# Performance work log

Measured on AMD Instinct MI355X. Metric: run time of the kernel, lower is better.

## Reference

```python
import jax, jax.numpy as jnp
import numpy as np


def setup_inputs() -> dict:
    key = jax.random.key(0)
    kq, kv = jax.random.split(key)
    N, To, Ti, H = 8, 1024, 4096, 512
    queries = jax.random.normal(kq, (N, To, H), dtype=jnp.float32)
    values = jax.random.normal(kv, (N, Ti, H), dtype=jnp.float32)
    return {"queries": queries, "values": values}


def reference(queries, values):
    # scores: N x To x Ti (unscaled, unmasked dot-product attention)
    scores = jnp.einsum("noh,nih->noi", queries, values)
    attn = jax.nn.softmax(scores, axis=-1)          # softmax over Ti
    out = jnp.einsum("noi,nih->noh", attn, values)  # N x To x H
    return out, attn
```

## Files before the change

### kernel.cpp

```cpp
#include <hip/hip_runtime.h>
#include <hip/hip_bf16.h>

typedef __bf16 bf16x8 __attribute__((ext_vector_type(8)));
typedef __bf16 bf16x4 __attribute__((ext_vector_type(4)));
typedef float  f32x4  __attribute__((ext_vector_type(4)));

constexpr int N_  = 8;
constexpr int TO_ = 1024;
constexpr int TI_ = 4096;
constexpr int H_  = 512;

__device__ inline void split8(const float4& x0, const float4& x1,
                              bf16x8& h, bf16x8& l)
{
    float xs[8] = {x0.x, x0.y, x0.z, x0.w, x1.x, x1.y, x1.z, x1.w};
#pragma unroll
    for (int i = 0; i < 8; ++i) {
        __bf16 hh = (__bf16)xs[i];
        h[i] = hh;
        l[i] = (__bf16)(xs[i] - (float)hh);
    }
}

__device__ inline void cvt8(const float4& x0, const float4& x1, bf16x8& h)
{
    float xs[8] = {x0.x, x0.y, x0.z, x0.w, x1.x, x1.y, x1.z, x1.w};
#pragma unroll
    for (int i = 0; i < 8; ++i) h[i] = (__bf16)xs[i];
}

__global__ __launch_bounds__(256)
void zero_kernel(float4* __restrict__ p)
{
    p[(size_t)blockIdx.x * 256 + threadIdx.x] = float4{0.f, 0.f, 0.f, 0.f};
}

__global__ __launch_bounds__(256)
void split_kernel(const float* __restrict__ X, __bf16* __restrict__ Xh,
                  __bf16* __restrict__ Xl)
{
    const size_t idx = ((size_t)blockIdx.x * 256 + threadIdx.x) * 8;
    const float4* src = reinterpret_cast<const float4*>(X + idx);
    float4 x0 = src[0], x1 = src[1];
    bf16x8 h, l;
    split8(x0, x1, h, l);
    *reinterpret_cast<bf16x8*>(Xh + idx) = h;
    *reinterpret_cast<bf16x8*>(Xl + idx) = l;
}

__global__ __launch_bounds__(256)
void vt2_kernel(const __bf16* __restrict__ Vh, __bf16* __restrict__ Vt)
{
    const int hb = blockIdx.x, tb = blockIdx.y, n = blockIdx.z;
    const int h  = hb * 64 + (threadIdx.x >> 2);
    const int tq = threadIdx.x & 3;
    const __bf16* Vn = Vh + (size_t)n * TI_ * H_;
    __bf16* Vtn = Vt + (size_t)n * H_ * TI_;

#pragma unroll
    for (int j = 0; j < 16; ++j) {
        const int t0 = tb * 512 + tq * 128 + j * 8;
        bf16x8 o;
#pragma unroll
        for (int e = 0; e < 8; ++e)
            o[e] = Vn[(size_t)(t0 + e) * H_ + h];
        *reinterpret_cast<bf16x8*>(&Vtn[(size_t)h * TI_ + t0]) = o;
    }
}

constexpr int QLP = 40;

__global__ __launch_bounds__(256, 3)
void qk2_kernel(const __bf16* __restrict__ Qh, const __bf16* __restrict__ Ql,
                const __bf16* __restrict__ Vh, const __bf16* __restrict__ Vl,
                float* __restrict__ S)
{
    __shared__ __bf16 Ah[128 * QLP];
    __shared__ __bf16 Al[128 * QLP];
    __shared__ __bf16 Bh[128 * QLP];
    __shared__ __bf16 Bl[128 * QLP];

    const int tt = blockIdx.x, mt = blockIdx.y, n = blockIdx.z;
    const size_t qoff = ((size_t)n * TO_ + (size_t)mt * 128) * H_;
    const size_t voff = ((size_t)n * TI_ + (size_t)tt * 128) * H_;
    const __bf16* Qhb = Qh + qoff;
    const __bf16* Qlb = Ql + qoff;
    const __bf16* Vhb = Vh + voff;
    const __bf16* Vlb = Vl + voff;

    const int tid  = threadIdx.x;
    const int lane = tid & 63, wave = tid >> 6;
    const int wr = wave >> 1, wc = wave & 1;

    const int sr = tid >> 1;
    const int sc = (tid & 1) * 16;

    bf16x8 pAh[2], pAl[2], pBh[2], pBl[2];
    auto loadT = [&](int k0) {
#pragma unroll
        for (int c = 0; c < 2; ++c) {
            const size_t o = (size_t)sr * H_ + k0 + sc + c * 8;
            pAh[c] = *reinterpret_cast<const bf16x8*>(Qhb + o);
            pAl[c] = *reinterpret_cast<const bf16x8*>(Qlb + o);
            pBh[c] = *reinterpret_cast<const bf16x8*>(Vhb + o);
            pBl[c] = *reinterpret_cast<const bf16x8*>(Vlb + o);
        }
    };

    f32x4 acc[4][4] = {};
    const int fr = lane & 15, fg = (lane >> 4) * 8;

    loadT(0);
    for (int kt = 0; kt < 16; ++kt) {
        __syncthreads();
#pragma unroll
        for (int c = 0; c < 2; ++c) {
            const int o = sr * QLP + sc + c * 8;
            *reinterpret_cast<bf16x8*>(&Ah[o]) = pAh[c];
            *reinterpret_cast<bf16x8*>(&Al[o]) = pAl[c];
            *reinterpret_cast<bf16x8*>(&Bh[o]) = pBh[c];
            *reinterpret_cast<bf16x8*>(&Bl[o]) = pBl[c];
        }
        __syncthreads();
        if (kt + 1 < 16) loadT((kt + 1) * 32);

        bf16x8 bh[4], bl[4];
#pragma unroll
        for (int j = 0; j < 4; ++j) {
            const int row = wc * 64 + j * 16 + fr;
            bh[j] = *reinterpret_cast<const bf16x8*>(&Bh[row * QLP + fg]);
            bl[j] = *reinterpret_cast<const bf16x8*>(&Bl[row * QLP + fg]);
        }
#pragma unroll
        for (int m = 0; m < 4; ++m) {
            const int row = wr * 64 + m * 16 + fr;
            bf16x8 ah = *reinterpret_cast<const bf16x8*>(&Ah[row * QLP + fg]);
            bf16x8 al = *reinterpret_cast<const bf16x8*>(&Al[row * QLP + fg]);
#pragma unroll
            for (int j = 0; j < 4; ++j) {
                acc[m][j] = __builtin_amdgcn_mfma_f32_16x16x32_bf16(ah, bh[j], acc[m][j], 0, 0, 0);
                acc[m][j] = __builtin_amdgcn_mfma_f32_16x16x32_bf16(ah, bl[j], acc[m][j], 0, 0, 0);
                acc[m][j] = __builtin_amdgcn_mfma_f32_16x16x32_bf16(al, bh[j], acc[m][j], 0, 0, 0);
            }
        }
    }

    float* Sb = S + ((size_t)n * TO_ + (size_t)mt * 128) * TI_ + (size_t)tt * 128;
    const int crow0 = wr * 64 + (lane >> 4) * 4;
    const int ccol0 = wc * 64 + (lane & 15);
#pragma unroll
    for (int m = 0; m < 4; ++m)
#pragma unroll
        for (int j = 0; j < 4; ++j)
#pragma unroll
            for (int r = 0; r < 4; ++r)
                Sb[(size_t)(crow0 + m * 16 + r) * TI_ + (ccol0 + j * 16)] = acc[m][j][r];
}

__global__ __launch_bounds__(256)
void softmax2_kernel(float* __restrict__ S, __bf16* __restrict__ A16)
{
    const int wave = threadIdx.x >> 6, lane = threadIdx.x & 63;
    const size_t row = (size_t)blockIdx.x * 4 + wave;
    float4* p = reinterpret_cast<float4*>(S + row * TI_);
    __bf16* p16 = A16 + row * TI_;

    float4 v[16];
    float m = -3.0e38f;
#pragma unroll
    for (int j = 0; j < 16; ++j) {
        v[j] = p[j * 64 + lane];
        m = fmaxf(m, fmaxf(fmaxf(v[j].x, v[j].y), fmaxf(v[j].z, v[j].w)));
    }
#pragma unroll
    for (int s = 32; s > 0; s >>= 1) m = fmaxf(m, __shfl_xor(m, s));

    constexpr float L2E = 1.4426950408889634f;
    float sum = 0.f;
#pragma unroll
    for (int j = 0; j < 16; ++j) {
        v[j].x = exp2f((v[j].x - m) * L2E);
        v[j].y = exp2f((v[j].y - m) * L2E);
        v[j].z = exp2f((v[j].z - m) * L2E);
        v[j].w = exp2f((v[j].w - m) * L2E);
        sum += (v[j].x + v[j].y) + (v[j].z + v[j].w);
    }
#pragma unroll
    for (int s = 32; s > 0; s >>= 1) sum += __shfl_xor(sum, s);

    const float inv = 1.0f / sum;
#pragma unroll
    for (int j = 0; j < 16; ++j) {
        v[j].x *= inv; v[j].y *= inv; v[j].z *= inv; v[j].w *= inv;
        p[j * 64 + lane] = v[j];
        bf16x4 o;
        o[0] = (__bf16)v[j].x; o[1] = (__bf16)v[j].y;
        o[2] = (__bf16)v[j].z; o[3] = (__bf16)v[j].w;
        *reinterpret_cast<bf16x4*>(&p16[(j * 64 + lane) * 4]) = o;
    }
}

constexpr int VBM = 128, VBN = 256, VBK = 64, VKC = 1024;

__global__ __launch_bounds__(256, 2)
void pv6_kernel(const __bf16* __restrict__ A16, const __bf16* __restrict__ Vt,
                float* __restrict__ O)
{
    __shared__ __bf16 Asm[VBM * VBK];
    __shared__ __bf16 Bsm[VBN * VBK];

    const int flat = blockIdx.x;
    const int mt = flat >> 6;
    const int g  = flat & 63;
    const int n  = g >> 3;
    const int ht = (g >> 2) & 1;
    const int kc = g & 3;

    const __bf16* Ab = A16 + ((size_t)n * TO_ + (size_t)mt * VBM) * TI_ + (size_t)kc * VKC;
    const __bf16* Bb = Vt  + ((size_t)n * H_  + (size_t)ht * VBN) * TI_ + (size_t)kc * VKC;

    const int tid = threadIdx.x, lane = tid & 63, wave = tid >> 6;
    const int wm = wave >> 1, wh = wave & 1;
    const int fr = lane & 15, fq = lane >> 4;

    f32x4 acc[4][8] = {};

    for (int kt = 0; kt < VKC / VBK; ++kt) {
        const int k0 = kt * VBK;
        __syncthreads();

#pragma unroll
        for (int i = 0; i < 4; ++i) {
            const int q   = i * 256 + tid;
            const int row = q >> 3, c = q & 7;
            const int csw = c ^ (row & 7);
            const __bf16* gs = Ab + (size_t)row * TI_ + k0 + csw * 8;
            const int q0 = i * 256 + wave * 64;
            __builtin_amdgcn_global_load_lds(
                (const __attribute__((address_space(1))) void*)gs,
                (__attribute__((address_space(3))) void*)((char*)Asm + q0 * 16),
                16, 0, 0);
        }
#pragma unroll
        for (int i = 0; i < 8; ++i) {
            const int q   = i * 256 + tid;
            const int row = q >> 3, c = q & 7;
            const int csw = c ^ (row & 7);
            const __bf16* gs = Bb + (size_t)row * TI_ + k0 + csw * 8;
            const int q0 = i * 256 + wave * 64;
            __builtin_amdgcn_global_load_lds(
                (const __attribute__((address_space(1))) void*)gs,
                (__attribute__((address_space(3))) void*)((char*)Bsm + q0 * 16),
                16, 0, 0);
        }
        __syncthreads();

#pragma unroll
        for (int kk = 0; kk < 2; ++kk) {
            bf16x8 a[4], b[8];
#pragma unroll
            for (int m = 0; m < 4; ++m) {
                const int row = wm * 64 + m * 16 + fr;
                const int cph = (kk * 4 + fq) ^ (row & 7);
                a[m] = *reinterpret_cast<const bf16x8*>(
                    (const char*)Asm + row * 128 + cph * 16);
            }
#pragma unroll
            for (int j = 0; j < 8; ++j) {
                const int row = wh * 128 + j * 16 + fr;
                const int cph = (kk * 4 + fq) ^ (row & 7);
                b[j] = *reinterpret_cast<const bf16x8*>(
                    (const char*)Bsm + row * 128 + cph * 16);
            }
#pragma unroll
            for (int m = 0; m < 4; ++m)
#pragma unroll
                for (int j = 0; j < 8; ++j)
                    acc[m][j] = __builtin_amdgcn_mfma_f32_16x16x32_bf16(
                        a[m], b[j], acc[m][j], 0, 0, 0);
        }
    }

    float* Ob = O + ((size_t)n * TO_ + (size_t)mt * VBM) * H_ + ht * VBN;
#pragma unroll
    for (int m = 0; m < 4; ++m) {
        const int orow = wm * 64 + m * 16 + fq * 4;
#pragma unroll
        for (int j = 0; j < 8; ++j) {
            const int ocol = wh * 128 + j * 16 + fr;
#pragma unroll
            for (int r = 0; r < 4; ++r)
                atomicAdd(&Ob[(size_t)(orow + r) * H_ + ocol], acc[m][j][r]);
        }
    }
}

constexpr int BM1 = 128, BN1 = 128, BK1 = 32, LP1 = BK1 + 8;

__global__ __launch_bounds__(256, 2)
void qk_kernel(const float* __restrict__ Q, const float* __restrict__ V,
               float* __restrict__ S)
{
    __shared__ __bf16 Ah[BM1 * LP1];
    __shared__ __bf16 Al[BM1 * LP1];
    __shared__ __bf16 Bh[BN1 * LP1];
    __shared__ __bf16 Bl[BN1 * LP1];

    const int tt = blockIdx.x, mt = blockIdx.y, n = blockIdx.z;
    const float* Qb = Q + ((size_t)n * TO_ + (size_t)mt * BM1) * H_;
    const float* Vb = V + ((size_t)n * TI_ + (size_t)tt * BN1) * H_;

    const int tid  = threadIdx.x;
    const int lane = tid & 63, wave = tid >> 6;
    const int wr = wave >> 1, wc = wave & 1;
    const int srow = tid >> 2, scg = tid & 3;

    f32x4 acc[4][4] = {};

    for (int k0 = 0; k0 < H_; k0 += BK1) {
        __syncthreads();
#pragma unroll
        for (int half = 0; half < 2; ++half) {
            const int r = srow + half * 64;
            {
                const float4* src =
                    reinterpret_cast<const float4*>(Qb + (size_t)r * H_ + k0 + scg * 8);
                float4 x0 = src[0], x1 = src[1];
                bf16x8 hv, lv;
                split8(x0, x1, hv, lv);
                *reinterpret_cast<bf16x8*>(&Ah[r * LP1 + scg * 8]) = hv;
                *reinterpret_cast<bf16x8*>(&Al[r * LP1 + scg * 8]) = lv;
            }
            {
                const float4* src =
                    reinterpret_cast<const float4*>(Vb + (size_t)r * H_ + k0 + scg * 8);
                float4 x0 = src[0], x1 = src[1];
                bf16x8 hv, lv;
                split8(x0, x1, hv, lv);
                *reinterpret_cast<bf16x8*>(&Bh[r * LP1 + scg * 8]) = hv;
                *reinterpret_cast<bf16x8*>(&Bl[r * LP1 + scg * 8]) = lv;
            }
        }
        __syncthreads();

        bf16x8 ah[4], al[4], bh[4], bl[4];
        const int fr = lane & 15, fg = (lane >> 4) * 8;
#pragma unroll
        for (int m = 0; m < 4; ++m) {
            const int row = wr * 64 + m * 16 + fr;
            ah[m] = *reinterpret_cast<const bf16x8*>(&Ah[row * LP1 + fg]);
            al[m] = *reinterpret_cast<const bf16x8*>(&Al[row * LP1 + fg]);
        }
#pragma unroll
        for (int j = 0; j < 4; ++j) {
            const int row = wc * 64 + j * 16 + fr;
            bh[j] = *reinterpret_cast<const bf16x8*>(&Bh[row * LP1 + fg]);
            bl[j] = *reinterpret_cast<const bf16x8*>(&Bl[row * LP1 + fg]);
        }
#pragma unroll
        for (int m = 0; m < 4; ++m)
#pragma unroll
            for (int j = 0; j < 4; ++j) {
                acc[m][j] = __builtin_amdgcn_mfma_f32_16x16x32_bf16(ah[m], bh[j], acc[m][j], 0, 0, 0);
                acc[m][j] = __builtin_amdgcn_mfma_f32_16x16x32_bf16(ah[m], bl[j], acc[m][j], 0, 0, 0);
                acc[m][j] = __builtin_amdgcn_mfma_f32_16x16x32_bf16(al[m], bh[j], acc[m][j], 0, 0, 0);
            }
    }

    float* Sb = S + ((size_t)n * TO_ + (size_t)mt * BM1) * TI_ + (size_t)tt * BN1;
    const int crow0 = wr * 64 + (lane >> 4) * 4;
    const int ccol0 = wc * 64 + (lane & 15);
#pragma unroll
    for (int m = 0; m < 4; ++m)
#pragma unroll
        for (int j = 0; j < 4; ++j)
#pragma unroll
            for (int r = 0; r < 4; ++r)
                Sb[(size_t)(crow0 + m * 16 + r) * TI_ + (ccol0 + j * 16)] = acc[m][j][r];
}

__global__ __launch_bounds__(256)
void softmax_kernel(float* __restrict__ S)
{
    const int wave = threadIdx.x >> 6, lane = threadIdx.x & 63;
    const size_t row = (size_t)blockIdx.x * 4 + wave;
    float4* p = reinterpret_cast<float4*>(S + row * TI_);

    float4 v[16];
    float m = -3.0e38f;
#pragma unroll
    for (int j = 0; j < 16; ++j) {
        v[j] = p[j * 64 + lane];
        m = fmaxf(m, fmaxf(fmaxf(v[j].x, v[j].y), fmaxf(v[j].z, v[j].w)));
    }
#pragma unroll
    for (int s = 32; s > 0; s >>= 1) m = fmaxf(m, __shfl_xor(m, s));

    constexpr float L2E = 1.4426950408889634f;
    float sum = 0.f;
#pragma unroll
    for (int j = 0; j < 16; ++j) {
        v[j].x = exp2f((v[j].x - m) * L2E);
        v[j].y = exp2f((v[j].y - m) * L2E);
        v[j].z = exp2f((v[j].z - m) * L2E);
        v[j].w = exp2f((v[j].w - m) * L2E);
        sum += (v[j].x + v[j].y) + (v[j].z + v[j].w);
    }
#pragma unroll
    for (int s = 32; s > 0; s >>= 1) sum += __shfl_xor(sum, s);

    const float inv = 1.0f / sum;
#pragma unroll
    for (int j = 0; j < 16; ++j) {
        v[j].x *= inv; v[j].y *= inv; v[j].z *= inv; v[j].w *= inv;
        p[j * 64 + lane] = v[j];
    }
}

__global__ __launch_bounds__(256)
void vt_kernel(const float* __restrict__ V, __bf16* __restrict__ Vt)
{
    const int hb = blockIdx.x, tb = blockIdx.y, n = blockIdx.z;
    const int h  = hb * 64 + (threadIdx.x >> 2);
    const int tq = threadIdx.x & 3;
    const float* Vn = V + (size_t)n * TI_ * H_;
    __bf16* Vtn = Vt + (size_t)n * H_ * TI_;

#pragma unroll
    for (int j = 0; j < 16; ++j) {
        const int t0 = tb * 512 + tq * 128 + j * 8;
        bf16x8 o;
#pragma unroll
        for (int e = 0; e < 8; ++e)
            o[e] = (__bf16)Vn[(size_t)(t0 + e) * H_ + h];
        *reinterpret_cast<bf16x8*>(&Vtn[(size_t)h * TI_ + t0]) = o;
    }
}

constexpr int PBM = 32, PBK = 64, PLP = PBK + 8;

__global__ __launch_bounds__(512, 2)
void pv_fast_kernel(const float* __restrict__ A, const __bf16* __restrict__ Vt,
                    float* __restrict__ O)
{
    __shared__ __bf16 AsmF[PBM * PLP];
    __shared__ __bf16 BsmF[512 * PLP];

    const int n = blockIdx.x, mt = blockIdx.y;
    const float*  Ab = A  + ((size_t)n * TO_ + (size_t)mt * PBM) * TI_;
    const __bf16* Vb = Vt + (size_t)n * H_ * TI_;

    const int tid = threadIdx.x, lane = tid & 63, wv = tid >> 6;
    const int ar = tid >> 4;
    const int ac = (tid & 15) * 4;
    const int bh = tid >> 3;
    const int bc = (tid & 7) * 8;

    float4 aReg;
    bf16x8 bReg[8];

    auto loadTile = [&](int k0) {
        aReg = *reinterpret_cast<const float4*>(Ab + (size_t)ar * TI_ + k0 + ac);
#pragma unroll
        for (int i = 0; i < 8; ++i)
            bReg[i] = *reinterpret_cast<const bf16x8*>(
                Vb + (size_t)(bh + i * 64) * TI_ + k0 + bc);
    };

    f32x4 acc[2][4] = {};
    const int fr = lane & 15, fg = (lane >> 4) * 8;

    loadTile(0);
    constexpr int NT = TI_ / PBK;
    for (int kt = 0; kt < NT; ++kt) {
        __syncthreads();
        {
            bf16x4 av;
            av[0] = (__bf16)aReg.x; av[1] = (__bf16)aReg.y;
            av[2] = (__bf16)aReg.z; av[3] = (__bf16)aReg.w;
            *reinterpret_cast<bf16x4*>(&AsmF[ar * PLP + ac]) = av;
#pragma unroll
            for (int i = 0; i < 8; ++i)
                *reinterpret_cast<bf16x8*>(&BsmF[(bh + i * 64) * PLP + bc]) = bReg[i];
        }
        __syncthreads();
        if (kt + 1 < NT) loadTile((kt + 1) * PBK);

#pragma unroll
        for (int kk = 0; kk < 2; ++kk) {
            bf16x8 af[2], bfr[4];
#pragma unroll
            for (int m = 0; m < 2; ++m)
                af[m] = *reinterpret_cast<const bf16x8*>(
                    &AsmF[(m * 16 + fr) * PLP + kk * 32 + fg]);
#pragma unroll
            for (int j = 0; j < 4; ++j)
                bfr[j] = *reinterpret_cast<const bf16x8*>(
                    &BsmF[(wv * 64 + j * 16 + fr) * PLP + kk * 32 + fg]);
#pragma unroll
            for (int m = 0; m < 2; ++m)
#pragma unroll
                for (int j = 0; j < 4; ++j)
                    acc[m][j] = __builtin_amdgcn_mfma_f32_16x16x32_bf16(
                        af[m], bfr[j], acc[m][j], 0, 0, 0);
        }
    }

    float* Ob = O + ((size_t)n * TO_ + (size_t)mt * PBM) * H_ + wv * 64;
    const int crow = (lane >> 4) * 4;
    const int ccol = lane & 15;
#pragma unroll
    for (int m = 0; m < 2; ++m)
#pragma unroll
        for (int j = 0; j < 4; ++j)
#pragma unroll
            for (int r = 0; r < 4; ++r)
                Ob[(size_t)(m * 16 + crow + r) * H_ + j * 16 + ccol] = acc[m][j][r];
}

extern "C" void kernel_launch(void* const* d_in, const int* in_sizes, int n_in,
                              void* d_out, int out_size, void* d_ws, size_t ws_size,
                              hipStream_t stream)
{
    const float* Q = (const float*)d_in[0];
    const float* V = (const float*)d_in[1];
    float* out  = (float*)d_out;
    float* attn = out + (size_t)N_ * TO_ * H_;

    const size_t NV = (size_t)N_ * TI_ * H_;
    const size_t NQ = (size_t)N_ * TO_ * H_;
    const size_t FULL_BYTES = (3 * NV + 2 * NQ) * sizeof(__bf16);
    const size_t VT_BYTES   = NV * sizeof(__bf16);

    __bf16* wsb = (__bf16*)d_ws;
    __bf16* Vt = wsb;
    __bf16* Vh = wsb + NV;
    __bf16* Vl = wsb + 2 * NV;
    __bf16* Qh = wsb + 3 * NV;
    __bf16* Ql = wsb + 3 * NV + NQ;
    __bf16* A16 = wsb + NV;

    if (ws_size >= FULL_BYTES) {
        zero_kernel<<<dim3((unsigned)(NQ / 4 / 256)), 256, 0, stream>>>((float4*)out);
        split_kernel<<<dim3(NV / (256 * 8)), 256, 0, stream>>>(V, Vh, Vl);
        split_kernel<<<dim3(NQ / (256 * 8)), 256, 0, stream>>>(Q, Qh, Ql);
        vt2_kernel<<<dim3(H_ / 64, TI_ / 512, N_), 256, 0, stream>>>(Vh, Vt);
        qk2_kernel<<<dim3(TI_ / 128, TO_ / 128, N_), 256, 0, stream>>>(Qh, Ql, Vh, Vl, attn);
        softmax2_kernel<<<dim3(N_ * TO_ / 4), 256, 0, stream>>>(attn, A16);
        pv6_kernel<<<dim3(512), 256, 0, stream>>>(A16, Vt, out);
    } else if (ws_size >= VT_BYTES) {
        vt_kernel<<<dim3(H_ / 64, TI_ / 512, N_), 256, 0, stream>>>(V, Vt);
        qk_kernel<<<dim3(TI_ / BN1, TO_ / BM1, N_), 256, 0, stream>>>(Q, V, attn);
        softmax_kernel<<<dim3(N_ * TO_ / 4), 256, 0, stream>>>(attn);
        pv_fast_kernel<<<dim3(N_, TO_ / PBM), 512, 0, stream>>>(attn, Vt, out);
    }
}
```

Measured before the change: 296.0 us.

## Stage QK tiles with direct global-to-LDS loads and XOR-swizzled layout

Replaces the register-staged global-to-shared copies in the split-bf16 QK GEMM with direct global_load_lds transfers into XOR-swizzled shared memory. The K tile grows from 32 to 64, which halves the number of barrier pairs. The aim is to free VGPRs, cut the load/store instruction overhead and avoid LDS bank conflicts without padding. In exchange, shared memory doubles to 64KB per block and occupancy drops to 2 blocks per CU. Prefetch of the next tile during compute is also removed, so load latency is now exposed between the barriers.

After: 284.3 us. 1.04x faster.

```diff
diff --git a/kernel.cpp b/kernel.cpp
--- a/kernel.cpp
+++ b/kernel.cpp
@@ -68,17 +68,15 @@
     }
 }
 
-constexpr int QLP = 40;
-
-__global__ __launch_bounds__(256, 3)
-void qk2_kernel(const __bf16* __restrict__ Qh, const __bf16* __restrict__ Ql,
+__global__ __launch_bounds__(256, 2)
+void qk3_kernel(const __bf16* __restrict__ Qh, const __bf16* __restrict__ Ql,
                 const __bf16* __restrict__ Vh, const __bf16* __restrict__ Vl,
                 float* __restrict__ S)
 {
-    __shared__ __bf16 Ah[128 * QLP];
-    __shared__ __bf16 Al[128 * QLP];
-    __shared__ __bf16 Bh[128 * QLP];
-    __shared__ __bf16 Bl[128 * QLP];
+    __shared__ __bf16 Ah[128 * 64];
+    __shared__ __bf16 Al[128 * 64];
+    __shared__ __bf16 Bh[128 * 64];
+    __shared__ __bf16 Bl[128 * 64];
 
     const int tt = blockIdx.x, mt = blockIdx.y, n = blockIdx.z;
     const size_t qoff = ((size_t)n * TO_ + (size_t)mt * 128) * H_;
@@ -91,63 +89,67 @@
     const int tid  = threadIdx.x;
     const int lane = tid & 63, wave = tid >> 6;
     const int wr = wave >> 1, wc = wave & 1;
-
-    const int sr = tid >> 1;
-    const int sc = (tid & 1) * 16;
-
-    bf16x8 pAh[2], pAl[2], pBh[2], pBl[2];
-    auto loadT = [&](int k0) {
-#pragma unroll
-        for (int c = 0; c < 2; ++c) {
-            const size_t o = (size_t)sr * H_ + k0 + sc + c * 8;
-            pAh[c] = *reinterpret_cast<const bf16x8*>(Qhb + o);
-            pAl[c] = *reinterpret_cast<const bf16x8*>(Qlb + o);
-            pBh[c] = *reinterpret_cast<const bf16x8*>(Vhb + o);
-            pBl[c] = *reinterpret_cast<const bf16x8*>(Vlb + o);
+    const int fr = lane & 15, fq = lane >> 4;
+
+    const int srow = tid >> 3;
+    const int sc   = tid & 7;
+
+    auto stage = [&](const __bf16* __restrict__ g, __bf16* lds, int k0) {
+#pragma unroll
+        for (int i = 0; i < 4; ++i) {
+            const int row = i * 32 + srow;
+            const int csw = sc ^ (row & 7);
+            const __bf16* gs = g + (size_t)row * H_ + k0 + csw * 8;
+            const int q0 = (i * 256 + wave * 64) * 16;
+            __builtin_amdgcn_global_load_lds(
+                (const __attribute__((address_space(1))) void*)gs,
+                (__attribute__((address_space(3))) void*)((char*)lds + q0),
+                16, 0, 0);
         }
     };
 
     f32x4 acc[4][4] = {};
-    const int fr = lane & 15, fg = (lane >> 4) * 8;
-
-    loadT(0);
-    for (int kt = 0; kt < 16; ++kt) {
-        __syncthreads();
-#pragma unroll
-        for (int c = 0; c < 2; ++c) {
-            const int o = sr * QLP + sc + c * 8;
-            *reinterpret_cast<bf16x8*>(&Ah[o]) = pAh[c];
-            *reinterpret_cast<bf16x8*>(&Al[o]) = pAl[c];
-            *reinterpret_cast<bf16x8*>(&Bh[o]) = pBh[c];
-            *reinterpret_cast<bf16x8*>(&Bl[o]) = pBl[c];
-        }
-        __syncthreads();
-        if (kt + 1 < 16) loadT((kt + 1) * 32);
-
-        bf16x8 bh[4], bl[4];
-#pragma unroll
-        for (int j = 0; j < 4; ++j) {
-            const int row = wc * 64 + j * 16 + fr;
-            bh[j] = *reinterpret_cast<const bf16x8*>(&Bh[row * QLP + fg]);
-            bl[j] = *reinterpret_cast<const bf16x8*>(&Bl[row * QLP + fg]);
-        }
-#pragma unroll
-        for (int m = 0; m < 4; ++m) {
-            const int row = wr * 64 + m * 16 + fr;
-            bf16x8 ah = *reinterpret_cast<const bf16x8*>(&Ah[row * QLP + fg]);
-            bf16x8 al = *reinterpret_cast<const bf16x8*>(&Al[row * QLP + fg]);
+
+    for (int kt = 0; kt < H_ / 64; ++kt) {
+        const int k0 = kt * 64;
+        __syncthreads();
+        stage(Qhb, Ah, k0);
+        stage(Qlb, Al, k0);
+        stage(Vhb, Bh, k0);
+        stage(Vlb, Bl, k0);
+        __syncthreads();
+
+#pragma unroll
+        for (int kk = 0; kk < 2; ++kk) {
+            bf16x8 ah[4], al[4], bh[4], bl[4];
+#pragma unroll
+            for (int m = 0; m < 4; ++m) {
+                const int row = wr * 64 + m * 16 + fr;
+                const int cs  = (kk * 4 + fq) ^ (row & 7);
+                ah[m] = *reinterpret_cast<const bf16x8*>(&Ah[row * 64 + cs * 8]);
+                al[m] = *reinterpret_cast<const bf16x8*>(&Al[row * 64 + cs * 8]);
+            }
 #pragma unroll
             for (int j = 0; j < 4; ++j) {
-                acc[m][j] = __builtin_amdgcn_mfma_f32_16x16x32_bf16(ah, bh[j], acc[m][j], 0, 0, 0);
-                acc[m][j] = __builtin_amdgcn_mfma_f32_16x16x32_bf16(ah, bl[j], acc[m][j], 0, 0, 0);
-                acc[m][j] = __builtin_amdgcn_mfma_f32_16x16x32_bf16(al, bh[j], acc[m][j], 0, 0, 0);
-            }
+                const int row = wc * 64 + j * 16 + fr;
+                const int cs  = (kk * 4 + fq) ^ (row & 7);
+                bh[j] = *reinterpret_cast<const bf16x8*>(&Bh[row * 64 + cs * 8]);
+                bl[j] = *reinterpret_cast<const bf16x8*>(&Bl[row * 64 + cs * 8]);
+            }
+#pragma unroll
+            for (int m = 0; m < 4; ++m)
+#pragma unroll
+                for (int j = 0; j < 4; ++j) {
+                    acc[m][j] = __builtin_amdgcn_mfma_f32_16x16x32_bf16(ah[m], bh[j], acc[m][j], 0, 0, 0);
+                    acc[m][j] = __builtin_amdgcn_mfma_f32_16x16x32_bf16(ah[m], bl[j], acc[m][j], 0, 0, 0);
+                    acc[m][j] = __builtin_amdgcn_mfma_f32_16x16x32_bf16(al[m], bh[j], acc[m][j], 0, 0, 0);
+                }
         }
     }
 
     float* Sb = S + ((size_t)n * TO_ + (size_t)mt * 128) * TI_ + (size_t)tt * 128;
-    const int crow0 = wr * 64 + (lane >> 4) * 4;
-    const int ccol0 = wc * 64 + (lane & 15);
+    const int crow0 = wr * 64 + fq * 4;
+    const int ccol0 = wc * 64 + fr;
 #pragma unroll
     for (int m = 0; m < 4; ++m)
 #pragma unroll
@@ -545,7 +547,7 @@
         split_kernel<<<dim3(NV / (256 * 8)), 256, 0, stream>>>(V, Vh, Vl);
         split_kernel<<<dim3(NQ / (256 * 8)), 256, 0, stream>>>(Q, Qh, Ql);
         vt2_kernel<<<dim3(H_ / 64, TI_ / 512, N_), 256, 0, stream>>>(Vh, Vt);
-        qk2_kernel<<<dim3(TI_ / 128, TO_ / 128, N_), 256, 0, stream>>>(Qh, Ql, Vh, Vl, attn);
+        qk3_kernel<<<dim3(TI_ / 128, TO_ / 128, N_), 256, 0, stream>>>(Qh, Ql, Vh, Vl, attn);
         softmax2_kernel<<<dim3(N_ * TO_ / 4), 256, 0, stream>>>(attn, A16);
         pv6_kernel<<<dim3(512), 256, 0, stream>>>(A16, Vt, out);
     } else if (ws_size >= VT_BYTES) {
```
